# Optimization experiments

Hardware: AMD Instinct MI355X
Metric: run time of the kernel (lower is better)

Reference implementation:

```python
import jax, jax.numpy as jnp
import numpy as np

HEADS = 16

def setup_inputs() -> dict:
    key = jax.random.key(0)
    ks = jax.random.split(key, 8)
    B, Lq, G, Lkv, dim, dim_kv = 4, 512, 4, 1024, 1024, 1024
    inner = dim_kv  # dim_per_head * heads = (dim_kv // heads) * heads
    H = jax.random.normal(ks[0], (B, Lq, dim), dtype=jnp.float32)
    KV = jax.random.normal(ks[1], (B, G, Lkv, dim_kv), dtype=jnp.float32)
    KV_mask = jax.random.randint(ks[2], (B, G, Lkv), 0, 2, dtype=jnp.int32)
    s = 0.02
    Wq = jax.random.normal(ks[3], (dim, inner), dtype=jnp.float32) * s
    Wk = jax.random.normal(ks[4], (dim_kv, inner), dtype=jnp.float32) * s
    Wv = jax.random.normal(ks[5], (dim_kv, inner), dtype=jnp.float32) * s
    Wo = jax.random.normal(ks[6], (inner, dim), dtype=jnp.float32) * s
    return {"H": H, "KV": KV, "KV_mask": KV_mask,
            "Wq": Wq, "Wk": Wk, "Wv": Wv, "Wo": Wo}


def reference(H, KV, KV_mask, Wq, Wk, Wv, Wo):
    B, Lq, dim = H.shape
    _, G, Lkv, dim_kv = KV.shape
    inner = Wq.shape[1]
    h = HEADS
    d = inner // h

    # q: [B, h, Lq, d], pre-scaled as in the torch module
    q = (H @ Wq).reshape(B, Lq, h, d).transpose(0, 2, 1, 3) * (d ** -0.5)
    # k, v: [B, G, h, Lkv, d] -- all graphs batched instead of Python loop
    k = jnp.einsum('bgle,ef->bglf', KV, Wk).reshape(B, G, Lkv, h, d).transpose(0, 1, 3, 2, 4)
    v = jnp.einsum('bgle,ef->bglf', KV, Wv).reshape(B, G, Lkv, h, d).transpose(0, 1, 3, 2, 4)

    # scores: [B, G, h, Lq, Lkv]
    scores = jnp.einsum('bhqd,bghkd->bghqk', q, k)
    # additive mask: (1 - mask) * finfo.min, mask broadcast over heads & queries
    mask = KV_mask.astype(scores.dtype)  # [B, G, Lkv]
    scores = scores + (1.0 - mask)[:, :, None, None, :] * jnp.finfo(scores.dtype).min

    attn = jax.nn.softmax(scores.astype(jnp.float32), axis=-1).astype(scores.dtype)
    ctx = jnp.einsum('bghqk,bghkd->bghqd', attn, v)  # [B, G, h, Lq, d]
    ctx = ctx.transpose(0, 1, 3, 2, 4).reshape(B, G, Lq, inner)
    out = ctx @ Wo  # [B, G, Lq, dim]
    # concat over graphs along last dim, matching torch.cat(all_attn, dim=-1)
    out = out.transpose(0, 2, 1, 3).reshape(B, Lq, G * dim)
    return out
```

## Files before the change

### kernel.cpp

```cpp
#include <hip/hip_runtime.h>

using f16   = _Float16;
using f16x8 = _Float16 __attribute__((ext_vector_type(8)));
using f16x4 = _Float16 __attribute__((ext_vector_type(4)));
using f32x4 = float    __attribute__((ext_vector_type(4)));

constexpr int BM = 128, BN = 128, BK = 64;
constexpr int KD = 1024, ND = 1024;

__device__ __forceinline__ int swz(int r, int c) {
  return r * BK + ((c ^ (r & 7)) << 3);
}

__global__ __launch_bounds__(256)
void wtrans_k(const float* __restrict__ W, f16* __restrict__ Wt) {
  __shared__ float tile[32][33];
  int bx = blockIdx.x * 32;
  int by = blockIdx.y * 32;
  int tx = threadIdx.x, ty = threadIdx.y;
#pragma unroll
  for (int i = 0; i < 4; ++i) {
    int r = ty + i * 8;
    tile[r][tx] = W[(size_t)(by + r) * ND + bx + tx];
  }
  __syncthreads();
#pragma unroll
  for (int i = 0; i < 4; ++i) {
    int r = ty + i * 8;
    Wt[(size_t)(bx + r) * KD + by + tx] = (f16)tile[tx][r];
  }
}

template <int MODE>
__global__ __launch_bounds__(256)
void gemm_k(const float* __restrict__ A, const f16* __restrict__ Bt,
            void* __restrict__ C, float scale) {
  __shared__ __attribute__((aligned(16))) f16 As[BM * BK];
  __shared__ __attribute__((aligned(16))) f16 Bs[BN * BK];
  const int t = threadIdx.x;
  const int w = t >> 6, l = t & 63, l15 = l & 15, lg = l >> 4;
  const int m0 = blockIdx.y * BM, n0 = blockIdx.x * BN;
  const int wm = (w >> 1) * 64, wn = (w & 1) * 64;

  f32x4 acc[4][4] = {};

  for (int kb = 0; kb < KD; kb += BK) {
#pragma unroll
    for (int rr = 0; rr < 2; ++rr) {
      int idx = rr * 256 + t;
      int r = idx >> 2, q = idx & 3;
      const f32x4* src = (const f32x4*)(A + (size_t)(m0 + r) * KD + kb + q * 16);
      f16 bv[16];
#pragma unroll
      for (int i = 0; i < 4; ++i) {
        f32x4 x = src[i];
        bv[i * 4 + 0] = (f16)x[0]; bv[i * 4 + 1] = (f16)x[1];
        bv[i * 4 + 2] = (f16)x[2]; bv[i * 4 + 3] = (f16)x[3];
      }
      int c0 = q * 2;
      *(f16x8*)&As[swz(r, c0)]     = *(f16x8*)&bv[0];
      *(f16x8*)&As[swz(r, c0 + 1)] = *(f16x8*)&bv[8];
    }
#pragma unroll
    for (int rr = 0; rr < 4; ++rr) {
      int idx = rr * 256 + t;
      int r = idx >> 3, c = idx & 7;
      f16x8 x = *(const f16x8*)(Bt + (size_t)(n0 + r) * KD + kb + c * 8);
      *(f16x8*)&Bs[swz(r, c)] = x;
    }
    __syncthreads();
#pragma unroll
    for (int ks = 0; ks < 2; ++ks) {
      f16x8 av[4], bw[4];
      int cc = ks * 4 + lg;
#pragma unroll
      for (int mf = 0; mf < 4; ++mf)
        av[mf] = *(const f16x8*)&As[swz(wm + mf * 16 + l15, cc)];
#pragma unroll
      for (int nf = 0; nf < 4; ++nf)
        bw[nf] = *(const f16x8*)&Bs[swz(wn + nf * 16 + l15, cc)];
#pragma unroll
      for (int mf = 0; mf < 4; ++mf)
#pragma unroll
        for (int nf = 0; nf < 4; ++nf)
          acc[mf][nf] = __builtin_amdgcn_mfma_f32_16x16x32_f16(
              av[mf], bw[nf], acc[mf][nf], 0, 0, 0);
    }
    __syncthreads();
  }

#pragma unroll
  for (int mf = 0; mf < 4; ++mf) {
#pragma unroll
    for (int nf = 0; nf < 4; ++nf) {
      int mb = m0 + wm + mf * 16 + 4 * lg;
      int n  = n0 + wn + nf * 16 + l15;
      if (MODE == 0) {
#pragma unroll
        for (int r = 0; r < 4; ++r)
          ((f16*)C)[(size_t)(mb + r) * ND + n] = (f16)(acc[mf][nf][r] * scale);
      } else if (MODE == 1) {
        int bg = mb >> 10, kv = mb & 1023;
        int h = n >> 6, e = n & 63;
        f16x4 pk;
#pragma unroll
        for (int r = 0; r < 4; ++r) pk[r] = (f16)acc[mf][nf][r];
        *(f16x4*)((f16*)C + (size_t)((bg * 16 + h) * 64 + e) * 1024 + kv) = pk;
      } else {
#pragma unroll
        for (int r = 0; r < 4; ++r) {
          int m = mb + r;
          int bg = m >> 9, lq = m & 511;
          int bb = bg >> 2, g = bg & 3;
          ((float*)C)[(size_t)(((bb << 9) + lq) * 4 + g) * 1024 + n] =
              acc[mf][nf][r];
        }
      }
    }
  }
}

__global__ __launch_bounds__(256)
void attn_k(const f16* __restrict__ Qb, const f16* __restrict__ Kb,
            const f16* __restrict__ Vt, const int* __restrict__ mask,
            float* __restrict__ ctx) {
  __shared__ int smask[1024];
  __shared__ __attribute__((aligned(16))) f16 Ks[64 * 64];
  __shared__ __attribute__((aligned(16))) f16 Vs[64 * 64];
  __shared__ __attribute__((aligned(16))) f16 Pl[4][16 * 72];

  const int t = threadIdx.x, w = t >> 6, l = t & 63, l15 = l & 15, lg = l >> 4;
  const int y = blockIdx.y;
  const int bg = y >> 4, h = y & 15;
  const int bb = bg >> 2;
  const int q0 = blockIdx.x * 64 + w * 16;

  *(int4*)&smask[t * 4] = *(const int4*)(mask + bg * 1024 + t * 4);
  __syncthreads();

  f16x8 aQ[2];
  const f16* qp = Qb + (size_t)(bb * 512 + q0 + l15) * 1024 + h * 64 + lg * 8;
  aQ[0] = *(const f16x8*)qp;
  aQ[1] = *(const f16x8*)(qp + 32);

  float mrow[4], rs[4] = {0.f, 0.f, 0.f, 0.f};
#pragma unroll
  for (int r = 0; r < 4; ++r) mrow[r] = -1e30f;
  f32x4 accO[4] = {};

  const f16* Kbase = Kb + (size_t)bg * 1024 * 1024 + h * 64;
  const f16* Vbase = Vt + (size_t)(bg * 16 + h) * 64 * 1024;

  for (int c16 = 0; c16 < 16; ++c16) {
    const int kv0 = c16 * 64;
#pragma unroll
    for (int rr = 0; rr < 2; ++rr) {
      int idx = rr * 256 + t;
      int r = idx >> 3, cc = idx & 7;
      f16x8 kx = *(const f16x8*)(Kbase + (size_t)(kv0 + r) * 1024 + cc * 8);
      *(f16x8*)&Ks[swz(r, cc)] = kx;
      f16x8 vx = *(const f16x8*)(Vbase + (size_t)r * 1024 + kv0 + cc * 8);
      *(f16x8*)&Vs[swz(r, cc)] = vx;
    }
    __syncthreads();

    f32x4 s[4] = {};
#pragma unroll
    for (int nf = 0; nf < 4; ++nf) {
      int kr = nf * 16 + l15;
      f16x8 k0 = *(const f16x8*)&Ks[swz(kr, lg)];
      f16x8 k1 = *(const f16x8*)&Ks[swz(kr, 4 + lg)];
      s[nf] = __builtin_amdgcn_mfma_f32_16x16x32_f16(aQ[0], k0, s[nf], 0, 0, 0);
      s[nf] = __builtin_amdgcn_mfma_f32_16x16x32_f16(aQ[1], k1, s[nf], 0, 0, 0);
    }
#pragma unroll
    for (int nf = 0; nf < 4; ++nf) {
      if (smask[kv0 + nf * 16 + l15] == 0) {
#pragma unroll
        for (int r = 0; r < 4; ++r) s[nf][r] = -1e30f;
      }
    }
#pragma unroll
    for (int r = 0; r < 4; ++r) {
      float v = fmaxf(fmaxf(s[0][r], s[1][r]), fmaxf(s[2][r], s[3][r]));
      v = fmaxf(v, __shfl_xor(v, 1));
      v = fmaxf(v, __shfl_xor(v, 2));
      v = fmaxf(v, __shfl_xor(v, 4));
      v = fmaxf(v, __shfl_xor(v, 8));
      float mn = fmaxf(mrow[r], v);
      float sc = __expf(mrow[r] - mn);
      mrow[r] = mn;
      rs[r] *= sc;
#pragma unroll
      for (int nf = 0; nf < 4; ++nf) accO[nf][r] *= sc;
      float ps = 0.f;
#pragma unroll
      for (int nf = 0; nf < 4; ++nf) {
        float p = __expf(s[nf][r] - mn);
        ps += p;
        Pl[w][(4 * lg + r) * 72 + nf * 16 + l15] = (f16)p;
      }
      rs[r] += ps;
    }
#pragma unroll
    for (int ks = 0; ks < 2; ++ks) {
      f16x8 aP = *(const f16x8*)&Pl[w][l15 * 72 + ks * 32 + lg * 8];
#pragma unroll
      for (int nf = 0; nf < 4; ++nf) {
        f16x8 bV = *(const f16x8*)&Vs[swz(nf * 16 + l15, ks * 4 + lg)];
        accO[nf] = __builtin_amdgcn_mfma_f32_16x16x32_f16(aP, bV, accO[nf], 0, 0, 0);
      }
    }
    __syncthreads();
  }

#pragma unroll
  for (int r = 0; r < 4; ++r) {
    float v = rs[r];
    v += __shfl_xor(v, 1);
    v += __shfl_xor(v, 2);
    v += __shfl_xor(v, 4);
    v += __shfl_xor(v, 8);
    rs[r] = 1.0f / v;
  }
#pragma unroll
  for (int nf = 0; nf < 4; ++nf)
#pragma unroll
    for (int r = 0; r < 4; ++r) {
      int q = q0 + 4 * lg + r;
      ctx[(size_t)(bg * 512 + q) * 1024 + h * 64 + nf * 16 + l15] =
          accO[nf][r] * rs[r];
    }
}

extern "C" void kernel_launch(void* const* d_in, const int* in_sizes, int n_in,
                              void* d_out, int out_size, void* d_ws,
                              size_t ws_size, hipStream_t stream) {
  const float* H  = (const float*)d_in[0];
  const float* KV = (const float*)d_in[1];
  const int*  msk = (const int*)d_in[2];
  const float* Wq = (const float*)d_in[3];
  const float* Wk = (const float*)d_in[4];
  const float* Wv = (const float*)d_in[5];
  const float* Wo = (const float*)d_in[6];

  char* ws = (char*)d_ws;
  f16* WqT = (f16*)(ws + (size_t)0);
  f16* WkT = (f16*)(ws + ((size_t)2 << 20));
  f16* WvT = (f16*)(ws + ((size_t)4 << 20));
  f16* WoT = (f16*)(ws + ((size_t)6 << 20));
  f16* Qb  = (f16*)(ws + ((size_t)8 << 20));
  f16* Kb  = (f16*)(ws + ((size_t)12 << 20));
  f16* Vtb = (f16*)(ws + ((size_t)44 << 20));
  float* ctx = (float*)(ws + ((size_t)76 << 20));

  dim3 tb32(32, 8);
  wtrans_k<<<dim3(32, 32), tb32, 0, stream>>>(Wq, WqT);
  wtrans_k<<<dim3(32, 32), tb32, 0, stream>>>(Wk, WkT);
  wtrans_k<<<dim3(32, 32), tb32, 0, stream>>>(Wv, WvT);
  wtrans_k<<<dim3(32, 32), tb32, 0, stream>>>(Wo, WoT);

  gemm_k<0><<<dim3(8, 16),  256, 0, stream>>>(H,  WqT, (void*)Qb,  0.125f);
  gemm_k<0><<<dim3(8, 128), 256, 0, stream>>>(KV, WkT, (void*)Kb,  1.0f);
  gemm_k<1><<<dim3(8, 128), 256, 0, stream>>>(KV, WvT, (void*)Vtb, 1.0f);

  attn_k<<<dim3(8, 256), 256, 0, stream>>>(Qb, Kb, Vtb, msk, ctx);

  gemm_k<2><<<dim3(8, 64), 256, 0, stream>>>(ctx, WoT, d_out, 1.0f);
}
```

Measured before the change: 456.4 us.

## Pre-cast inputs to fp16, use direct global-to-LDS loads, widen attention query tile

```diff
diff --git a/kernel.cpp b/kernel.cpp
--- a/kernel.cpp
+++ b/kernel.cpp
@@ -10,6 +10,23 @@
 
 __device__ __forceinline__ int swz(int r, int c) {
   return r * BK + ((c ^ (r & 7)) << 3);
+}
+
+__device__ __forceinline__ void gload_lds16(const f16* g, f16* s) {
+  __builtin_amdgcn_global_load_lds(
+      (const __attribute__((address_space(1))) void*)g,
+      (__attribute__((address_space(3))) void*)s, 16, 0, 0);
+}
+
+__global__ __launch_bounds__(256)
+void cast_k(const float* __restrict__ in, f16* __restrict__ out) {
+  size_t i = ((size_t)blockIdx.x * 256 + threadIdx.x) * 8;
+  f32x4 a = *(const f32x4*)(in + i);
+  f32x4 b = *(const f32x4*)(in + i + 4);
+  f16x8 o;
+  o[0] = (f16)a[0]; o[1] = (f16)a[1]; o[2] = (f16)a[2]; o[3] = (f16)a[3];
+  o[4] = (f16)b[0]; o[5] = (f16)b[1]; o[6] = (f16)b[2]; o[7] = (f16)b[3];
+  *(f16x8*)(out + i) = o;
 }
 
 __global__ __launch_bounds__(256)
@@ -33,7 +50,7 @@
 
 template <int MODE>
 __global__ __launch_bounds__(256)
-void gemm_k(const float* __restrict__ A, const f16* __restrict__ Bt,
+void gemm_k(const f16* __restrict__ A, const f16* __restrict__ Bt,
             void* __restrict__ C, float scale) {
   __shared__ __attribute__((aligned(16))) f16 As[BM * BK];
   __shared__ __attribute__((aligned(16))) f16 Bs[BN * BK];
@@ -41,32 +58,21 @@
   const int w = t >> 6, l = t & 63, l15 = l & 15, lg = l >> 4;
   const int m0 = blockIdx.y * BM, n0 = blockIdx.x * BN;
   const int wm = (w >> 1) * 64, wn = (w & 1) * 64;
+  const int lr  = l >> 3;
+  const int csw = ((l & 7) ^ lr) << 3;
+
+  const f16* Ab = A  + (size_t)m0 * KD + csw;
+  const f16* Bb = Bt + (size_t)n0 * KD + csw;
 
   f32x4 acc[4][4] = {};
 
   for (int kb = 0; kb < KD; kb += BK) {
 #pragma unroll
-    for (int rr = 0; rr < 2; ++rr) {
-      int idx = rr * 256 + t;
-      int r = idx >> 2, q = idx & 3;
-      const f32x4* src = (const f32x4*)(A + (size_t)(m0 + r) * KD + kb + q * 16);
-      f16 bv[16];
-#pragma unroll
-      for (int i = 0; i < 4; ++i) {
-        f32x4 x = src[i];
-        bv[i * 4 + 0] = (f16)x[0]; bv[i * 4 + 1] = (f16)x[1];
-        bv[i * 4 + 2] = (f16)x[2]; bv[i * 4 + 3] = (f16)x[3];
-      }
-      int c0 = q * 2;
-      *(f16x8*)&As[swz(r, c0)]     = *(f16x8*)&bv[0];
-      *(f16x8*)&As[swz(r, c0 + 1)] = *(f16x8*)&bv[8];
-    }
-#pragma unroll
-    for (int rr = 0; rr < 4; ++rr) {
-      int idx = rr * 256 + t;
-      int r = idx >> 3, c = idx & 7;
-      f16x8 x = *(const f16x8*)(Bt + (size_t)(n0 + r) * KD + kb + c * 8);
-      *(f16x8*)&Bs[swz(r, c)] = x;
+    for (int i = 0; i < 4; ++i) {
+      int ii = w * 4 + i;
+      int r  = ii * 8 + lr;
+      gload_lds16(Ab + (size_t)r * KD + kb, &As[ii * 512]);
+      gload_lds16(Bb + (size_t)r * KD + kb, &Bs[ii * 512]);
     }
     __syncthreads();
 #pragma unroll
@@ -123,114 +129,135 @@
 __global__ __launch_bounds__(256)
 void attn_k(const f16* __restrict__ Qb, const f16* __restrict__ Kb,
             const f16* __restrict__ Vt, const int* __restrict__ mask,
-            float* __restrict__ ctx) {
+            f16* __restrict__ ctx) {
   __shared__ int smask[1024];
   __shared__ __attribute__((aligned(16))) f16 Ks[64 * 64];
   __shared__ __attribute__((aligned(16))) f16 Vs[64 * 64];
-  __shared__ __attribute__((aligned(16))) f16 Pl[4][16 * 72];
+  __shared__ __attribute__((aligned(16))) f16 Pl[4][32 * 72];
 
   const int t = threadIdx.x, w = t >> 6, l = t & 63, l15 = l & 15, lg = l >> 4;
-  const int y = blockIdx.y;
-  const int bg = y >> 4, h = y & 15;
-  const int bb = bg >> 2;
-  const int q0 = blockIdx.x * 64 + w * 16;
+  const int y = blockIdx.y, bg = y >> 4, h = y & 15, bb = bg >> 2;
+  const int q0 = blockIdx.x * 128 + w * 32;
+  const int lr = l >> 3, csw = ((l & 7) ^ lr) << 3;
 
   *(int4*)&smask[t * 4] = *(const int4*)(mask + bg * 1024 + t * 4);
+
+  f16x8 aQ[2][2];
+#pragma unroll
+  for (int mf = 0; mf < 2; ++mf) {
+    const f16* qp =
+        Qb + (size_t)(bb * 512 + q0 + mf * 16 + l15) * 1024 + h * 64 + lg * 8;
+    aQ[mf][0] = *(const f16x8*)qp;
+    aQ[mf][1] = *(const f16x8*)(qp + 32);
+  }
+
+  float mrow[2][4], rs[2][4];
+#pragma unroll
+  for (int mf = 0; mf < 2; ++mf)
+#pragma unroll
+    for (int r = 0; r < 4; ++r) { mrow[mf][r] = -1e30f; rs[mf][r] = 0.f; }
+  f32x4 accO[2][4] = {};
+
+  const f16* Kbase = Kb + (size_t)bg * (1024 * 1024) + h * 64 + csw;
+  const f16* Vbase = Vt + (size_t)(bg * 16 + h) * (64 * 1024) + csw;
+
   __syncthreads();
-
-  f16x8 aQ[2];
-  const f16* qp = Qb + (size_t)(bb * 512 + q0 + l15) * 1024 + h * 64 + lg * 8;
-  aQ[0] = *(const f16x8*)qp;
-  aQ[1] = *(const f16x8*)(qp + 32);
-
-  float mrow[4], rs[4] = {0.f, 0.f, 0.f, 0.f};
-#pragma unroll
-  for (int r = 0; r < 4; ++r) mrow[r] = -1e30f;
-  f32x4 accO[4] = {};
-
-  const f16* Kbase = Kb + (size_t)bg * 1024 * 1024 + h * 64;
-  const f16* Vbase = Vt + (size_t)(bg * 16 + h) * 64 * 1024;
 
   for (int c16 = 0; c16 < 16; ++c16) {
     const int kv0 = c16 * 64;
 #pragma unroll
-    for (int rr = 0; rr < 2; ++rr) {
-      int idx = rr * 256 + t;
-      int r = idx >> 3, cc = idx & 7;
-      f16x8 kx = *(const f16x8*)(Kbase + (size_t)(kv0 + r) * 1024 + cc * 8);
-      *(f16x8*)&Ks[swz(r, cc)] = kx;
-      f16x8 vx = *(const f16x8*)(Vbase + (size_t)r * 1024 + kv0 + cc * 8);
-      *(f16x8*)&Vs[swz(r, cc)] = vx;
+    for (int i = 0; i < 2; ++i) {
+      int ii = w * 2 + i;
+      int r  = ii * 8 + lr;
+      gload_lds16(Kbase + (size_t)(kv0 + r) * 1024, &Ks[ii * 512]);
+      gload_lds16(Vbase + (size_t)r * 1024 + kv0,   &Vs[ii * 512]);
     }
     __syncthreads();
 
-    f32x4 s[4] = {};
+    f32x4 s[2][4] = {};
 #pragma unroll
     for (int nf = 0; nf < 4; ++nf) {
       int kr = nf * 16 + l15;
       f16x8 k0 = *(const f16x8*)&Ks[swz(kr, lg)];
       f16x8 k1 = *(const f16x8*)&Ks[swz(kr, 4 + lg)];
-      s[nf] = __builtin_amdgcn_mfma_f32_16x16x32_f16(aQ[0], k0, s[nf], 0, 0, 0);
-      s[nf] = __builtin_amdgcn_mfma_f32_16x16x32_f16(aQ[1], k1, s[nf], 0, 0, 0);
+#pragma unroll
+      for (int mf = 0; mf < 2; ++mf) {
+        s[mf][nf] = __builtin_amdgcn_mfma_f32_16x16x32_f16(aQ[mf][0], k0, s[mf][nf], 0, 0, 0);
+        s[mf][nf] = __builtin_amdgcn_mfma_f32_16x16x32_f16(aQ[mf][1], k1, s[mf][nf], 0, 0, 0);
+      }
     }
 #pragma unroll
     for (int nf = 0; nf < 4; ++nf) {
       if (smask[kv0 + nf * 16 + l15] == 0) {
 #pragma unroll
-        for (int r = 0; r < 4; ++r) s[nf][r] = -1e30f;
-      }
-    }
-#pragma unroll
-    for (int r = 0; r < 4; ++r) {
-      float v = fmaxf(fmaxf(s[0][r], s[1][r]), fmaxf(s[2][r], s[3][r]));
-      v = fmaxf(v, __shfl_xor(v, 1));
-      v = fmaxf(v, __shfl_xor(v, 2));
-      v = fmaxf(v, __shfl_xor(v, 4));
-      v = fmaxf(v, __shfl_xor(v, 8));
-      float mn = fmaxf(mrow[r], v);
-      float sc = __expf(mrow[r] - mn);
-      mrow[r] = mn;
-      rs[r] *= sc;
-#pragma unroll
-      for (int nf = 0; nf < 4; ++nf) accO[nf][r] *= sc;
-      float ps = 0.f;
-#pragma unroll
-      for (int nf = 0; nf < 4; ++nf) {
-        float p = __expf(s[nf][r] - mn);
-        ps += p;
-        Pl[w][(4 * lg + r) * 72 + nf * 16 + l15] = (f16)p;
-      }
-      rs[r] += ps;
-    }
+        for (int mf = 0; mf < 2; ++mf)
+#pragma unroll
+          for (int r = 0; r < 4; ++r) s[mf][nf][r] = -1e30f;
+      }
+    }
+#pragma unroll
+    for (int mf = 0; mf < 2; ++mf)
+#pragma unroll
+      for (int r = 0; r < 4; ++r) {
+        float v = fmaxf(fmaxf(s[mf][0][r], s[mf][1][r]),
+                        fmaxf(s[mf][2][r], s[mf][3][r]));
+        v = fmaxf(v, __shfl_xor(v, 1));
+        v = fmaxf(v, __shfl_xor(v, 2));
+        v = fmaxf(v, __shfl_xor(v, 4));
+        v = fmaxf(v, __shfl_xor(v, 8));
+        float mn = fmaxf(mrow[mf][r], v);
+        float sc = __expf(mrow[mf][r] - mn);
+        mrow[mf][r] = mn;
+        rs[mf][r] *= sc;
+#pragma unroll
+        for (int nf = 0; nf < 4; ++nf) accO[mf][nf][r] *= sc;
+        float ps = 0.f;
+#pragma unroll
+        for (int nf = 0; nf < 4; ++nf) {
+          float p = __expf(s[mf][nf][r] - mn);
+          ps += p;
+          Pl[w][(mf * 16 + 4 * lg + r) * 72 + nf * 16 + l15] = (f16)p;
+        }
+        rs[mf][r] += ps;
+      }
 #pragma unroll
     for (int ks = 0; ks < 2; ++ks) {
-      f16x8 aP = *(const f16x8*)&Pl[w][l15 * 72 + ks * 32 + lg * 8];
+      f16x8 aP[2];
+#pragma unroll
+      for (int mf = 0; mf < 2; ++mf)
+        aP[mf] = *(const f16x8*)&Pl[w][(mf * 16 + l15) * 72 + ks * 32 + lg * 8];
 #pragma unroll
       for (int nf = 0; nf < 4; ++nf) {
         f16x8 bV = *(const f16x8*)&Vs[swz(nf * 16 + l15, ks * 4 + lg)];
-        accO[nf] = __builtin_amdgcn_mfma_f32_16x16x32_f16(aP, bV, accO[nf], 0, 0, 0);
+#pragma unroll
+        for (int mf = 0; mf < 2; ++mf)
+          accO[mf][nf] = __builtin_amdgcn_mfma_f32_16x16x32_f16(aP[mf], bV, accO[mf][nf], 0, 0, 0);
       }
     }
     __syncthreads();
   }
 
 #pragma unroll
-  for (int r = 0; r < 4; ++r) {
-    float v = rs[r];
-    v += __shfl_xor(v, 1);
-    v += __shfl_xor(v, 2);
-    v += __shfl_xor(v, 4);
-    v += __shfl_xor(v, 8);
-    rs[r] = 1.0f / v;
-  }
-#pragma unroll
-  for (int nf = 0; nf < 4; ++nf)
+  for (int mf = 0; mf < 2; ++mf)
 #pragma unroll
     for (int r = 0; r < 4; ++r) {
-      int q = q0 + 4 * lg + r;
-      ctx[(size_t)(bg * 512 + q) * 1024 + h * 64 + nf * 16 + l15] =
-          accO[nf][r] * rs[r];
-    }
+      float v = rs[mf][r];
+      v += __shfl_xor(v, 1);
+      v += __shfl_xor(v, 2);
+      v += __shfl_xor(v, 4);
+      v += __shfl_xor(v, 8);
+      rs[mf][r] = 1.0f / v;
+    }
+#pragma unroll
+  for (int mf = 0; mf < 2; ++mf)
+#pragma unroll
+    for (int nf = 0; nf < 4; ++nf)
+#pragma unroll
+      for (int r = 0; r < 4; ++r) {
+        int q = q0 + mf * 16 + 4 * lg + r;
+        ctx[(size_t)(bg * 512 + q) * 1024 + h * 64 + nf * 16 + l15] =
+            (f16)(accO[mf][nf][r] * rs[mf][r]);
+      }
 }
 
 extern "C" void kernel_launch(void* const* d_in, const int* in_sizes, int n_in,
@@ -245,14 +272,19 @@
   const float* Wo = (const float*)d_in[6];
 
   char* ws = (char*)d_ws;
-  f16* WqT = (f16*)(ws + (size_t)0);
-  f16* WkT = (f16*)(ws + ((size_t)2 << 20));
-  f16* WvT = (f16*)(ws + ((size_t)4 << 20));
-  f16* WoT = (f16*)(ws + ((size_t)6 << 20));
-  f16* Qb  = (f16*)(ws + ((size_t)8 << 20));
-  f16* Kb  = (f16*)(ws + ((size_t)12 << 20));
-  f16* Vtb = (f16*)(ws + ((size_t)44 << 20));
-  float* ctx = (float*)(ws + ((size_t)76 << 20));
+  f16* WqT  = (f16*)(ws + ((size_t)0  << 20));
+  f16* WkT  = (f16*)(ws + ((size_t)2  << 20));
+  f16* WvT  = (f16*)(ws + ((size_t)4  << 20));
+  f16* WoT  = (f16*)(ws + ((size_t)6  << 20));
+  f16* Hf   = (f16*)(ws + ((size_t)8  << 20));
+  f16* KVf  = (f16*)(ws + ((size_t)12 << 20));
+  f16* Qb   = (f16*)(ws + ((size_t)12 << 20));
+  f16* ctxf = (f16*)(ws + ((size_t)16 << 20));
+  f16* Kb   = (f16*)(ws + ((size_t)44 << 20));
+  f16* Vtb  = (f16*)(ws + ((size_t)76 << 20));
+
+  cast_k<<<1024, 256, 0, stream>>>(H,  Hf);
+  cast_k<<<8192, 256, 0, stream>>>(KV, KVf);
 
   dim3 tb32(32, 8);
   wtrans_k<<<dim3(32, 32), tb32, 0, stream>>>(Wq, WqT);
@@ -260,11 +292,11 @@
   wtrans_k<<<dim3(32, 32), tb32, 0, stream>>>(Wv, WvT);
   wtrans_k<<<dim3(32, 32), tb32, 0, stream>>>(Wo, WoT);
 
-  gemm_k<0><<<dim3(8, 16),  256, 0, stream>>>(H,  WqT, (void*)Qb,  0.125f);
-  gemm_k<0><<<dim3(8, 128), 256, 0, stream>>>(KV, WkT, (void*)Kb,  1.0f);
-  gemm_k<1><<<dim3(8, 128), 256, 0, stream>>>(KV, WvT, (void*)Vtb, 1.0f);
-
-  attn_k<<<dim3(8, 256), 256, 0, stream>>>(Qb, Kb, Vtb, msk, ctx);
-
-  gemm_k<2><<<dim3(8, 64), 256, 0, stream>>>(ctx, WoT, d_out, 1.0f);
-}
+  gemm_k<0><<<dim3(8, 128), 256, 0, stream>>>(KVf, WkT, (void*)Kb,  1.0f);
+  gemm_k<1><<<dim3(8, 128), 256, 0, stream>>>(KVf, WvT, (void*)Vtb, 1.0f);
+  gemm_k<0><<<dim3(8, 16),  256, 0, stream>>>(Hf,  WqT, (void*)Qb,  0.125f);
+
+  attn_k<<<dim3(4, 256), 256, 0, stream>>>(Qb, Kb, Vtb, msk, ctxf);
+
+  gemm_k<2><<<dim3(8, 64), 256, 0, stream>>>(ctxf, WoT, d_out, 1.0f);
+}
```

Result: faster. 403.9 us (-11.5%).
